# Kernel optimization log

Measured on AMD Instinct MI355X. Metric: run time of the kernel, lower is better.

Reference implementation:

```python
import jax, jax.numpy as jnp
import numpy as np

B, S, D, H, DK = 2, 2048, 1024, 16, 64
NUM_BUCKETS, MAX_DIST = 32, 128
EPS = 1e-6


def _relative_position_bucket(rel, num_buckets=NUM_BUCKETS, max_distance=MAX_DIST):
    # bidirectional (T5 encoder) bucketing
    nb = num_buckets // 2
    bucket = (rel > 0).astype(jnp.int32) * nb
    n = jnp.abs(rel)
    max_exact = nb // 2
    is_small = n < max_exact
    large = max_exact + (
        jnp.log(jnp.maximum(n, 1).astype(jnp.float32) / max_exact)
        / np.log(max_distance / max_exact)
        * (nb - max_exact)
    ).astype(jnp.int32)
    large = jnp.minimum(large, nb - 1)
    return bucket + jnp.where(is_small, n, large)


def softmax1(logits):
    # off-by-one softmax: exp(x-m) / (sum(exp(x-m)) + exp(-m))
    m = jax.lax.stop_gradient(jnp.max(logits, axis=-1, keepdims=True))
    e = jnp.exp(logits - m)
    return e / (jnp.sum(e, axis=-1, keepdims=True) + jnp.exp(-m))


def setup_inputs() -> dict:
    key = jax.random.key(0)
    ks = jax.random.split(key, 8)
    scale = 0.02
    return {
        "hidden_states": jax.random.normal(ks[0], (B, S, D), dtype=jnp.float32),
        "delete_gate_mask": jax.random.normal(ks[1], (B, S, 1), dtype=jnp.float32),
        "ln_w": jnp.ones((D,), dtype=jnp.float32),
        "q_w": jax.random.normal(ks[2], (D, H * DK), dtype=jnp.float32) * scale,
        "k_w": jax.random.normal(ks[3], (D, H * DK), dtype=jnp.float32) * scale,
        "v_w": jax.random.normal(ks[4], (D, H * DK), dtype=jnp.float32) * scale,
        "o_w": jax.random.normal(ks[5], (H * DK, D), dtype=jnp.float32) * scale,
        "rel_emb": jax.random.normal(ks[6], (NUM_BUCKETS, H), dtype=jnp.float32) * scale,
    }


def reference(hidden_states, delete_gate_mask, ln_w, q_w, k_w, v_w, o_w, rel_emb):
    # T5LayerNorm (RMS norm, no mean subtraction, no bias)
    var = jnp.mean(jnp.square(hidden_states), axis=-1, keepdims=True)
    x = hidden_states * jax.lax.rsqrt(var + EPS) * ln_w

    # projections (T5 Linear layers have no bias, no 1/sqrt(d) scaling)
    q = (x @ q_w).reshape(B, S, H, DK).transpose(0, 2, 1, 3)  # bhqd
    k = (x @ k_w).reshape(B, S, H, DK).transpose(0, 2, 1, 3)  # bhkd
    v = (x @ v_w).reshape(B, S, H, DK).transpose(0, 2, 1, 3)  # bhkd

    scores = jnp.einsum("bhqd,bhkd->bhqk", q, k)

    # relative position bias: [1, H, S, S]
    pos = jnp.arange(S)
    rel = pos[None, :] - pos[:, None]  # key_pos - query_pos
    bucket = _relative_position_bucket(rel)  # [S, S]
    position_bias = rel_emb[bucket].transpose(2, 0, 1)[None]  # [1,H,S,S]

    # delete gate: [B,S,1] -> additive mask over key axis [B,1,1,S]
    gate = delete_gate_mask[..., 0][:, None, None, :]

    scores = scores + position_bias + gate
    attn = softmax1(scores.astype(jnp.float32)).astype(scores.dtype)

    attn_out = jnp.einsum("bhqk,bhkd->bhqd", attn, v)
    attn_out = attn_out.transpose(0, 2, 1, 3).reshape(B, S, H * DK) @ o_w

    # residual (dropout disabled at p=0)
    return hidden_states + attn_out
```

## Files before the change

### kernel.cpp

```cpp
#include <hip/hip_runtime.h>
#include <hip/hip_bf16.h>
#include <math.h>

typedef __attribute__((ext_vector_type(8))) short short8;
typedef __attribute__((ext_vector_type(4))) float f32x4;

#define S_LEN   2048
#define DMODEL  1024
#define NHEAD   16
#define HDK     64
#define NBATCH  2
#define MTOT    (NBATCH*S_LEN)
#define LOG2E   1.4426950408889634f

__device__ __forceinline__ unsigned short f2bf(float f) {
  union { float f; unsigned u; } c; c.f = f;
  unsigned r = c.u + 0x7FFFu + ((c.u >> 16) & 1u);
  return (unsigned short)(r >> 16);
}

__device__ __forceinline__ short8 lds_ld16(const unsigned short* p) {
  return *reinterpret_cast<const short8*>(p);
}

__device__ __forceinline__ void gload_lds16(const unsigned short* g, unsigned short* l) {
  __builtin_amdgcn_global_load_lds(
      (const __attribute__((address_space(1))) unsigned int*)g,
      (__attribute__((address_space(3))) unsigned int*)l, 16, 0, 0);
}

__global__ __launch_bounds__(256) void transpose_w_kernel(
    const float* __restrict__ qw, const float* __restrict__ kw,
    const float* __restrict__ vw, const float* __restrict__ ow,
    unsigned short* __restrict__ wqkv, unsigned short* __restrict__ wo) {
  int z = blockIdx.z;
  const float* src = (z==0)?qw:(z==1)?kw:(z==2)?vw:ow;
  unsigned short* dst = (z<3) ? (wqkv + (size_t)z*DMODEL*DMODEL) : wo;
  __shared__ float tile[32][33];
  int n0 = blockIdx.x*32, k0 = blockIdx.y*32;
  int tx = threadIdx.x, ty = threadIdx.y;
  for (int r = ty; r < 32; r += 8)
    tile[r][tx] = src[(size_t)(k0+r)*DMODEL + n0 + tx];
  __syncthreads();
  for (int r = ty; r < 32; r += 8)
    dst[(size_t)(n0+r)*DMODEL + k0 + tx] = f2bf(tile[tx][r]);
}

__global__ void bias_table_kernel(const float* __restrict__ rel_emb,
                                  float* __restrict__ btab) {
  int idx = blockIdx.x*256 + threadIdx.x;
  if (idx >= NHEAD*4095) return;
  int h = idx / 4095, rp = idx % 4095, rel = rp - 2047;
  int bucket = (rel > 0) ? 16 : 0;
  int n = (rel < 0) ? -rel : rel;
  int v;
  if (n < 8) v = n;
  else {
    float lrv = logf((float)n * 0.125f) / 2.7725887f * 8.0f;
    v = 8 + (int)lrv;
    if (v > 15) v = 15;
  }
  btab[idx] = rel_emb[(size_t)(bucket + v)*NHEAD + h] * LOG2E;
}

__global__ void eg_kernel(const float* __restrict__ gmask,
                          float* __restrict__ egf,
                          unsigned short* __restrict__ egb) {
  int i = blockIdx.x*256 + threadIdx.x;
  float e = __expf(gmask[i]);
  egf[i] = e;
  egb[i] = f2bf(e);
}

__global__ __launch_bounds__(256) void rmsnorm_kernel(
    const float* __restrict__ hs, const float* __restrict__ lnw,
    unsigned short* __restrict__ xo) {
  int row = blockIdx.x, t = threadIdx.x;
  const float4 v = ((const float4*)(hs + (size_t)row*DMODEL))[t];
  float ss = v.x*v.x + v.y*v.y + v.z*v.z + v.w*v.w;
  #pragma unroll
  for (int off = 32; off >= 1; off >>= 1) ss += __shfl_xor(ss, off, 64);
  __shared__ float wsum[4];
  if ((t & 63) == 0) wsum[t >> 6] = ss;
  __syncthreads();
  float tot = wsum[0] + wsum[1] + wsum[2] + wsum[3];
  float sc = rsqrtf(tot * (1.0f/DMODEL) + 1e-6f);
  const float4 lw = ((const float4*)lnw)[t];
  uint2 o;
  o.x = (unsigned)f2bf(v.x*sc*lw.x) | ((unsigned)f2bf(v.y*sc*lw.y) << 16);
  o.y = (unsigned)f2bf(v.z*sc*lw.z) | ((unsigned)f2bf(v.w*sc*lw.w) << 16);
  ((uint2*)(xo + (size_t)row*DMODEL))[t] = o;
}

template<int EPI>
__global__ __launch_bounds__(256) void gemm128(
    const unsigned short* __restrict__ X,
    const unsigned short* __restrict__ W,
    unsigned short* __restrict__ Oq, unsigned short* __restrict__ Ok,
    unsigned short* __restrict__ Ov,
    const float* __restrict__ resid, float* __restrict__ Of,
    const float* __restrict__ escale) {
  __shared__ unsigned short As[128*64];
  __shared__ unsigned short Bs[128*64];
  const int z = blockIdx.z;
  int m0, n0;
  const unsigned short *Ap, *Bp;
  if (EPI == 0 && z == 2) {
    m0 = blockIdx.y*128; n0 = blockIdx.x*128;
    Ap = W + (size_t)2*DMODEL*DMODEL; Bp = X;
  } else {
    m0 = blockIdx.x*128; n0 = blockIdx.y*128;
    Ap = X; Bp = W + ((EPI==0) ? (size_t)z*DMODEL*DMODEL : 0);
  }
  const int t = threadIdx.x, lane = t & 63, w = t >> 6;
  const int g = lane >> 4, lr = lane & 15;
  const int wr = (w >> 1)*64, wc = (w & 1)*64;

  f32x4 acc[4][4];
  #pragma unroll
  for (int mi = 0; mi < 4; mi++)
    #pragma unroll
    for (int ni = 0; ni < 4; ni++) acc[mi][ni] = (f32x4){0.f,0.f,0.f,0.f};

  const unsigned short* ag[4]; const unsigned short* bg[4];
  unsigned short* al[4]; unsigned short* bl[4];
  #pragma unroll
  for (int i = 0; i < 4; i++) {
    int slot = t + i*256, row = slot >> 3, c8 = slot & 7;
    int cs = c8 ^ (row & 7);
    ag[i] = Ap + (size_t)(m0 + row)*DMODEL + cs*8;
    bg[i] = Bp + (size_t)(n0 + row)*DMODEL + cs*8;
    al[i] = As + slot*8;
    bl[i] = Bs + slot*8;
  }

  for (int kk = 0; kk < DMODEL; kk += 64) {
    #pragma unroll
    for (int i = 0; i < 4; i++) {
      gload_lds16(ag[i] + kk, al[i]);
      gload_lds16(bg[i] + kk, bl[i]);
    }
    __syncthreads();
    #pragma unroll
    for (int ks = 0; ks < 2; ks++) {
      short8 af[4], bfr[4];
      #pragma unroll
      for (int mi = 0; mi < 4; mi++) {
        int R = wr + mi*16 + lr;
        af[mi] = lds_ld16(As + R*64 + (((ks*4 + g) ^ (R & 7)) << 3));
      }
      #pragma unroll
      for (int ni = 0; ni < 4; ni++) {
        int R = wc + ni*16 + lr;
        bfr[ni] = lds_ld16(Bs + R*64 + (((ks*4 + g) ^ (R & 7)) << 3));
      }
      #pragma unroll
      for (int mi = 0; mi < 4; mi++)
        #pragma unroll
        for (int ni = 0; ni < 4; ni++)
          acc[mi][ni] = __builtin_amdgcn_mfma_f32_16x16x32_bf16(af[mi], bfr[ni], acc[mi][ni], 0, 0, 0);
    }
    __syncthreads();
  }

  if (EPI == 0) {
    if (z < 2) {
      unsigned short* dst = (z == 0) ? Oq : Ok;
      const float osc = (z == 0) ? LOG2E : 1.0f;
      #pragma unroll
      for (int mi = 0; mi < 4; mi++) {
        #pragma unroll
        for (int r = 0; r < 4; r++) {
          int m = m0 + wr + mi*16 + g*4 + r;
          int b = m >> 11, s = m & (S_LEN-1);
          unsigned short* drow = dst + ((size_t)b*NHEAD*S_LEN + s)*HDK;
          #pragma unroll
          for (int ni = 0; ni < 4; ni++) {
            int n = n0 + wc + ni*16 + lr;
            int h = n >> 6, dcol = n & 63;
            drow[(size_t)h*S_LEN*HDK + dcol] = f2bf(acc[mi][ni][r] * osc);
          }
        }
      }
    } else {
      #pragma unroll
      for (int ni = 0; ni < 4; ni++) {
        int n = n0 + wc + ni*16 + lr;
        int b = n >> 11, s = n & (S_LEN-1);
        float e = escale[n];
        #pragma unroll
        for (int mi = 0; mi < 4; mi++)
          #pragma unroll
          for (int r = 0; r < 4; r++) {
            int m = m0 + wr + mi*16 + g*4 + r;
            Ov[((size_t)b*DMODEL + m)*S_LEN + s] = f2bf(acc[mi][ni][r] * e);
          }
      }
    }
  } else {
    #pragma unroll
    for (int mi = 0; mi < 4; mi++) {
      #pragma unroll
      for (int r = 0; r < 4; r++) {
        int m = m0 + wr + mi*16 + g*4 + r;
        const float* rrow = resid + (size_t)m*DMODEL;
        float* orow = Of + (size_t)m*DMODEL;
        #pragma unroll
        for (int ni = 0; ni < 4; ni++) {
          int n = n0 + wc + ni*16 + lr;
          orow[n] = rrow[n] + acc[mi][ni][r];
        }
      }
    }
  }
}

__global__ __launch_bounds__(256, 2) void attn_kernel(
    const unsigned short* __restrict__ Qg,
    const unsigned short* __restrict__ Kg,
    const unsigned short* __restrict__ Vtg,
    const float* __restrict__ btab,
    const unsigned short* __restrict__ egb,
    unsigned short* __restrict__ Og) {
  __shared__ __align__(16) unsigned short Kl[2][64][64];
  __shared__ __align__(16) unsigned short Vl[2][64][64];
  __shared__ __align__(16) unsigned short Pl[4][16*64];

  const int flat = blockIdx.x;
  const int xcd = flat & 7, j = flat >> 3;
  const int bh = xcd*4 + (j >> 4), qx = j & 15;
  const int b = bh >> 4, h = bh & 15;
  const int q0 = qx * 128;

  const int t = threadIdx.x, w = t >> 6, lane = t & 63;
  const int g = lane >> 4, lr = lane & 15, l7 = lane & 7;
  const int srow0 = t >> 3, sg0 = t & 7, srow1 = srow0 + 32;
  const int swz = (sg0 ^ (srow0 & 7)) << 3;

  const unsigned short* Qb = Qg  + (size_t)bh*S_LEN*HDK;
  const unsigned short* Kb = Kg  + (size_t)bh*S_LEN*HDK;
  const unsigned short* Vb = Vtg + (size_t)bh*HDK*S_LEN;
  const unsigned short* ge = egb + (size_t)b*S_LEN;

  const int qs0A = q0 + w*32, qs0B = qs0A + 16;
  short8 qfA0 = *reinterpret_cast<const short8*>(Qb + (size_t)(qs0A+lr)*HDK + g*8);
  short8 qfA1 = *reinterpret_cast<const short8*>(Qb + (size_t)(qs0A+lr)*HDK + 32 + g*8);
  short8 qfB0 = *reinterpret_cast<const short8*>(Qb + (size_t)(qs0B+lr)*HDK + g*8);
  short8 qfB1 = *reinterpret_cast<const short8*>(Qb + (size_t)(qs0B+lr)*HDK + 32 + g*8);

  f32x4 accA[4], accB[4], l4A, l4B;
  #pragma unroll
  for (int n = 0; n < 4; n++) { accA[n] = (f32x4){0.f,0.f,0.f,0.f}; accB[n] = (f32x4){0.f,0.f,0.f,0.f}; }
  l4A = (f32x4){0.f,0.f,0.f,0.f}; l4B = (f32x4){0.f,0.f,0.f,0.f};

  const float* btb = btab + (size_t)h*4095 + 2047;
  const float cpos = btb[91];
  const float cneg = btb[-91];

  {
    *reinterpret_cast<uint4*>(&Kl[0][srow0][swz]) =
        *reinterpret_cast<const uint4*>(Kb + (size_t)srow0*HDK + sg0*8);
    *reinterpret_cast<uint4*>(&Kl[0][srow1][swz]) =
        *reinterpret_cast<const uint4*>(Kb + (size_t)srow1*HDK + sg0*8);
    *reinterpret_cast<uint4*>(&Vl[0][srow0][swz]) =
        *reinterpret_cast<const uint4*>(Vb + (size_t)srow0*S_LEN + sg0*8);
    *reinterpret_cast<uint4*>(&Vl[0][srow1][swz]) =
        *reinterpret_cast<const uint4*>(Vb + (size_t)srow1*S_LEN + sg0*8);
  }

  char* prow = (char*)&Pl[w][0] + lr*128;

  int cur = 0;
  const int NT = S_LEN/64;
  for (int kt = 0; kt < NT; ++kt) {
    const int key0 = kt*64;
    __syncthreads();

    uint4 nk0, nk1, nv0, nv1;
    const bool pf = (kt + 1 < NT);
    if (pf) {
      nk0 = *reinterpret_cast<const uint4*>(Kb + (size_t)(key0+64+srow0)*HDK + sg0*8);
      nk1 = *reinterpret_cast<const uint4*>(Kb + (size_t)(key0+64+srow1)*HDK + sg0*8);
      nv0 = *reinterpret_cast<const uint4*>(Vb + (size_t)srow0*S_LEN + key0+64 + sg0*8);
      nv1 = *reinterpret_cast<const uint4*>(Vb + (size_t)srow1*S_LEN + key0+64 + sg0*8);
    }

    short8 bk[4][2];
    #pragma unroll
    for (int n = 0; n < 4; n++) {
      const unsigned short* kr = &Kl[cur][n*16 + lr][0];
      bk[n][0] = lds_ld16(kr + ((g ^ l7) << 3));
      bk[n][1] = lds_ld16(kr + (((4 + g) ^ l7) << 3));
    }
    short8 bv[2][4];
    #pragma unroll
    for (int c = 0; c < 2; c++)
      #pragma unroll
      for (int n = 0; n < 4; n++)
        bv[c][n] = lds_ld16(&Vl[cur][n*16 + lr][((4*c + g) ^ l7) << 3]);
    short8 gv[2];
    #pragma unroll
    for (int c = 0; c < 2; c++) {
      short8 z8 = (short8){0,0,0,0,0,0,0,0};
      if (lr == 0)
        z8 = *reinterpret_cast<const short8*>(ge + key0 + c*32 + g*8);
      gv[c] = z8;
    }

#define PROCESS_SET(qf0_, qf1_, qs0_, acc_, l4_)                                      \
    {                                                                                 \
      const int dband = key0 - (qs0_);                                                \
      const bool band = (dband > -154 && dband < 106);                                \
      const float cc = band ? 0.f : ((dband > 0) ? cpos : cneg);                      \
      f32x4 zc = (f32x4){cc, cc, cc, cc};               \
      f32x4 sv[4];                                                                    \
      __builtin_amdgcn_s_setprio(1);                                                  \
      _Pragma("unroll") for (int n = 0; n < 4; n++) {                                 \
        sv[n] = __builtin_amdgcn_mfma_f32_16x16x32_bf16(bk[n][0], qf0_, zc, 0, 0, 0); \
        sv[n] = __builtin_amdgcn_mfma_f32_16x16x32_bf16(bk[n][1], qf1_, sv[n], 0, 0, 0); \
      }                                                                               \
      __builtin_amdgcn_s_setprio(0);                                                  \
      if (band) {                                                                     \
        const float* btq = btb + (dband - lr);                                        \
        _Pragma("unroll") for (int n = 0; n < 4; n++)                                 \
          _Pragma("unroll") for (int r = 0; r < 4; r++)                               \
            sv[n][r] += btq[n*16 + g*4 + r];                                          \
      }                                                                               \
      _Pragma("unroll") for (int n = 0; n < 4; n++)                                   \
        _Pragma("unroll") for (int r = 0; r < 4; r++)                                 \
          sv[n][r] = exp2f(sv[n][r]);                                                 \
      _Pragma("unroll") for (int n = 0; n < 4; n++) {                                 \
        unsigned plo_, phi_;                                                          \
        asm("v_cvt_pk_bf16_f32 %0, %1, %2" : "=v"(plo_) : "v"(sv[n][0]), "v"(sv[n][1])); \
        asm("v_cvt_pk_bf16_f32 %0, %1, %2" : "=v"(phi_) : "v"(sv[n][2]), "v"(sv[n][3])); \
        uint2 pw_; pw_.x = plo_; pw_.y = phi_;                                        \
        *reinterpret_cast<uint2*>(prow + ((((2*n + (g>>1)) ^ l7) << 4) + ((g & 1) << 3))) = pw_; \
      }                                                                               \
      __builtin_amdgcn_s_setprio(1);                                                  \
      _Pragma("unroll") for (int c = 0; c < 2; c++) {                                 \
        short8 pa_ = lds_ld16((const unsigned short*)(prow + (((4*c + g) ^ l7) << 4))); \
        _Pragma("unroll") for (int n = 0; n < 4; n++)                                 \
          acc_[n] = __builtin_amdgcn_mfma_f32_16x16x32_bf16(pa_, bv[c][n], acc_[n], 0, 0, 0); \
        l4_ = __builtin_amdgcn_mfma_f32_16x16x32_bf16(pa_, gv[c], l4_, 0, 0, 0);      \
      }                                                                               \
      __builtin_amdgcn_s_setprio(0);                                                  \
    }

    PROCESS_SET(qfA0, qfA1, qs0A, accA, l4A)
    PROCESS_SET(qfB0, qfB1, qs0B, accB, l4B)
#undef PROCESS_SET

    if (pf) {
      *reinterpret_cast<uint4*>(&Kl[cur^1][srow0][swz]) = nk0;
      *reinterpret_cast<uint4*>(&Kl[cur^1][srow1][swz]) = nk1;
      *reinterpret_cast<uint4*>(&Vl[cur^1][srow0][swz]) = nv0;
      *reinterpret_cast<uint4*>(&Vl[cur^1][srow1][swz]) = nv1;
    }
    cur ^= 1;
  }

#define FINAL_SET(acc_, l4_, qs0_)                                                    \
  {                                                                                   \
    _Pragma("unroll") for (int r = 0; r < 4; r++) {                                   \
      float lq = __shfl(l4_[r], g*16);                                                \
      float inv = 1.0f / (lq + 1.0f);                                                 \
      int srw = (qs0_) + g*4 + r;                                                     \
      unsigned short* orow = Og + ((size_t)b*S_LEN + srw)*DMODEL + h*HDK;             \
      _Pragma("unroll") for (int n = 0; n < 4; n++)                                   \
        orow[n*16 + lr] = f2bf(acc_[n][r] * inv);                                     \
    }                                                                                 \
  }
  FINAL_SET(accA, l4A, qs0A)
  FINAL_SET(accB, l4B, qs0B)
#undef FINAL_SET
}

extern "C" void kernel_launch(void* const* d_in, const int* in_sizes, int n_in,
                              void* d_out, int out_size, void* d_ws, size_t ws_size,
                              hipStream_t stream) {
  const float* hs   = (const float*)d_in[0];
  const float* gate = (const float*)d_in[1];
  const float* lnw  = (const float*)d_in[2];
  const float* qw   = (const float*)d_in[3];
  const float* kw   = (const float*)d_in[4];
  const float* vw   = (const float*)d_in[5];
  const float* ow   = (const float*)d_in[6];
  const float* rel  = (const float*)d_in[7];
  float* out = (float*)d_out;

  char* ws = (char*)d_ws;
  const size_t MB = 1ull << 20;
  unsigned short* xbf  = (unsigned short*)(ws);
  unsigned short* wqkv = (unsigned short*)(ws + 8*MB);
  unsigned short* wo   = (unsigned short*)(ws + 14*MB);
  unsigned short* qb   = (unsigned short*)(ws + 16*MB);
  unsigned short* kb   = (unsigned short*)(ws + 24*MB);
  unsigned short* vt   = (unsigned short*)(ws + 32*MB);
  unsigned short* ao   = (unsigned short*)(ws + 40*MB);
  float*          btab = (float*)(ws + 48*MB);
  float*          egf  = (float*)(ws + 48*MB + 256*1024);
  unsigned short* egb  = (unsigned short*)(ws + 48*MB + 272*1024);

  transpose_w_kernel<<<dim3(32,32,4), dim3(32,8), 0, stream>>>(qw, kw, vw, ow, wqkv, wo);
  bias_table_kernel<<<dim3(256), dim3(256), 0, stream>>>(rel, btab);
  eg_kernel<<<dim3(16), dim3(256), 0, stream>>>(gate, egf, egb);
  rmsnorm_kernel<<<dim3(MTOT), dim3(256), 0, stream>>>(hs, lnw, xbf);
  gemm128<0><<<dim3(MTOT/128, DMODEL/128, 3), dim3(256), 0, stream>>>(
      xbf, wqkv, qb, kb, vt, nullptr, nullptr, egf);
  attn_kernel<<<dim3(512), dim3(256), 0, stream>>>(
      qb, kb, vt, btab, egb, ao);
  gemm128<1><<<dim3(MTOT/128, DMODEL/128, 1), dim3(256), 0, stream>>>(
      ao, wo, nullptr, nullptr, nullptr, hs, out, nullptr);
}
```

Baseline: 138.4 us.

## Split attention over key halves with combine kernel and async LDS staging

Attention now splits the key range into two halves, doubling the grid to 1024 blocks and writing unnormalized partial outputs plus partial row sums. A new combine kernel adds the halves and normalizes. This is valid without rescaling because the kernel uses no running max. K/V staging switches to direct global-to-LDS loads, and the A/B query sets are interleaved in shared MFMA loops. In exchange it adds an extra launch, extra global traffic, and bf16 rounding of the partials. The split path runs only when the workspace is large enough.

Measured after the change: 142.7 us. 3.1% more time.

```diff
diff --git a/kernel.cpp b/kernel.cpp
--- a/kernel.cpp
+++ b/kernel.cpp
@@ -17,6 +17,10 @@
   union { float f; unsigned u; } c; c.f = f;
   unsigned r = c.u + 0x7FFFu + ((c.u >> 16) & 1u);
   return (unsigned short)(r >> 16);
+}
+__device__ __forceinline__ float bf2f(unsigned short u) {
+  union { unsigned u; float f; } c; c.u = ((unsigned)u) << 16;
+  return c.f;
 }
 
 __device__ __forceinline__ short8 lds_ld16(const unsigned short* p) {
@@ -215,32 +219,53 @@
   }
 }
 
+__global__ __launch_bounds__(256, 2) void combine_guard_dummy() {}
+template<int SPLIT>
 __global__ __launch_bounds__(256, 2) void attn_kernel(
     const unsigned short* __restrict__ Qg,
     const unsigned short* __restrict__ Kg,
     const unsigned short* __restrict__ Vtg,
     const float* __restrict__ btab,
     const unsigned short* __restrict__ egb,
-    unsigned short* __restrict__ Og) {
+    unsigned short* __restrict__ Og,
+    unsigned short* __restrict__ Op0,
+    unsigned short* __restrict__ Op1,
+    float* __restrict__ lpart) {
   __shared__ __align__(16) unsigned short Kl[2][64][64];
   __shared__ __align__(16) unsigned short Vl[2][64][64];
-  __shared__ __align__(16) unsigned short Pl[4][16*64];
+  __shared__ __align__(16) unsigned short Pl[4][2][16*64];
 
   const int flat = blockIdx.x;
   const int xcd = flat & 7, j = flat >> 3;
-  const int bh = xcd*4 + (j >> 4), qx = j & 15;
+  int bh, qx, half;
+  if (SPLIT) { bh = xcd*4 + (j >> 5); int rest = j & 31; qx = rest >> 1; half = rest & 1; }
+  else       { bh = xcd*4 + (j >> 4); qx = j & 15; half = 0; }
   const int b = bh >> 4, h = bh & 15;
   const int q0 = qx * 128;
+  const int ktbase = SPLIT ? half*16 : 0;
+  const int ktend  = SPLIT ? ktbase + 16 : 32;
 
   const int t = threadIdx.x, w = t >> 6, lane = t & 63;
   const int g = lane >> 4, lr = lane & 15, l7 = lane & 7;
-  const int srow0 = t >> 3, sg0 = t & 7, srow1 = srow0 + 32;
-  const int swz = (sg0 ^ (srow0 & 7)) << 3;
 
   const unsigned short* Qb = Qg  + (size_t)bh*S_LEN*HDK;
   const unsigned short* Kb = Kg  + (size_t)bh*S_LEN*HDK;
   const unsigned short* Vb = Vtg + (size_t)bh*HDK*S_LEN;
   const unsigned short* ge = egb + (size_t)b*S_LEN;
+
+  const int srow = t >> 3, sg0 = t & 7;
+  const int cs = sg0 ^ (srow & 7);
+  const unsigned short* kS0 = Kb + (size_t)srow*HDK + cs*8;
+  const unsigned short* kS1 = Kb + (size_t)(srow+32)*HDK + cs*8;
+  const unsigned short* vS0 = Vb + (size_t)srow*S_LEN + cs*8;
+  const unsigned short* vS1 = Vb + (size_t)(srow+32)*S_LEN + cs*8;
+
+#define STAGE(nb_, key_) do {                                          \
+    gload_lds16(kS0 + (size_t)(key_)*HDK, &Kl[nb_][0][0] + t*8);       \
+    gload_lds16(kS1 + (size_t)(key_)*HDK, &Kl[nb_][0][0] + t*8 + 2048);\
+    gload_lds16(vS0 + (key_),             &Vl[nb_][0][0] + t*8);       \
+    gload_lds16(vS1 + (key_),             &Vl[nb_][0][0] + t*8 + 2048);\
+  } while (0)
 
   const int qs0A = q0 + w*32, qs0B = qs0A + 16;
   short8 qfA0 = *reinterpret_cast<const short8*>(Qb + (size_t)(qs0A+lr)*HDK + g*8);
@@ -257,47 +282,17 @@
   const float cpos = btb[91];
   const float cneg = btb[-91];
 
-  {
-    *reinterpret_cast<uint4*>(&Kl[0][srow0][swz]) =
-        *reinterpret_cast<const uint4*>(Kb + (size_t)srow0*HDK + sg0*8);
-    *reinterpret_cast<uint4*>(&Kl[0][srow1][swz]) =
-        *reinterpret_cast<const uint4*>(Kb + (size_t)srow1*HDK + sg0*8);
-    *reinterpret_cast<uint4*>(&Vl[0][srow0][swz]) =
-        *reinterpret_cast<const uint4*>(Vb + (size_t)srow0*S_LEN + sg0*8);
-    *reinterpret_cast<uint4*>(&Vl[0][srow1][swz]) =
-        *reinterpret_cast<const uint4*>(Vb + (size_t)srow1*S_LEN + sg0*8);
-  }
-
-  char* prow = (char*)&Pl[w][0] + lr*128;
-
+  char* prowA = (char*)&Pl[w][0][0] + lr*128;
+  char* prowB = (char*)&Pl[w][1][0] + lr*128;
+
+  STAGE(0, ktbase*64);
   int cur = 0;
-  const int NT = S_LEN/64;
-  for (int kt = 0; kt < NT; ++kt) {
+  for (int kt = ktbase; kt < ktend; ++kt) {
     const int key0 = kt*64;
     __syncthreads();
 
-    uint4 nk0, nk1, nv0, nv1;
-    const bool pf = (kt + 1 < NT);
-    if (pf) {
-      nk0 = *reinterpret_cast<const uint4*>(Kb + (size_t)(key0+64+srow0)*HDK + sg0*8);
-      nk1 = *reinterpret_cast<const uint4*>(Kb + (size_t)(key0+64+srow1)*HDK + sg0*8);
-      nv0 = *reinterpret_cast<const uint4*>(Vb + (size_t)srow0*S_LEN + key0+64 + sg0*8);
-      nv1 = *reinterpret_cast<const uint4*>(Vb + (size_t)srow1*S_LEN + key0+64 + sg0*8);
-    }
-
-    short8 bk[4][2];
-    #pragma unroll
-    for (int n = 0; n < 4; n++) {
-      const unsigned short* kr = &Kl[cur][n*16 + lr][0];
-      bk[n][0] = lds_ld16(kr + ((g ^ l7) << 3));
-      bk[n][1] = lds_ld16(kr + (((4 + g) ^ l7) << 3));
-    }
-    short8 bv[2][4];
-    #pragma unroll
-    for (int c = 0; c < 2; c++)
-      #pragma unroll
-      for (int n = 0; n < 4; n++)
-        bv[c][n] = lds_ld16(&Vl[cur][n*16 + lr][((4*c + g) ^ l7) << 3]);
+    if (kt + 1 < ktend) STAGE(cur^1, key0+64);
+
     short8 gv[2];
     #pragma unroll
     for (int c = 0; c < 2; c++) {
@@ -307,72 +302,133 @@
       gv[c] = z8;
     }
 
-#define PROCESS_SET(qf0_, qf1_, qs0_, acc_, l4_)                                      \
+    const int dbA = key0 - qs0A, dbB = key0 - qs0B;
+    const bool bandA = (dbA > -154 && dbA < 106);
+    const bool bandB = (dbB > -154 && dbB < 106);
+    const float ccA = bandA ? 0.f : ((dbA > 0) ? cpos : cneg);
+    const float ccB = bandB ? 0.f : ((dbB > 0) ? cpos : cneg);
+    f32x4 svA[4], svB[4];
+    {
+      f32x4 zA = (f32x4){ccA,ccA,ccA,ccA}, zB = (f32x4){ccB,ccB,ccB,ccB};
+      short8 bk[4];
+      #pragma unroll
+      for (int n = 0; n < 4; n++)
+        bk[n] = lds_ld16(&Kl[cur][n*16 + lr][(g ^ l7) << 3]);
+      __builtin_amdgcn_s_setprio(1);
+      #pragma unroll
+      for (int n = 0; n < 4; n++) {
+        svA[n] = __builtin_amdgcn_mfma_f32_16x16x32_bf16(bk[n], qfA0, zA, 0, 0, 0);
+        svB[n] = __builtin_amdgcn_mfma_f32_16x16x32_bf16(bk[n], qfB0, zB, 0, 0, 0);
+      }
+      __builtin_amdgcn_s_setprio(0);
+      #pragma unroll
+      for (int n = 0; n < 4; n++)
+        bk[n] = lds_ld16(&Kl[cur][n*16 + lr][((4 + g) ^ l7) << 3]);
+      __builtin_amdgcn_s_setprio(1);
+      #pragma unroll
+      for (int n = 0; n < 4; n++) {
+        svA[n] = __builtin_amdgcn_mfma_f32_16x16x32_bf16(bk[n], qfA1, svA[n], 0, 0, 0);
+        svB[n] = __builtin_amdgcn_mfma_f32_16x16x32_bf16(bk[n], qfB1, svB[n], 0, 0, 0);
+      }
+      __builtin_amdgcn_s_setprio(0);
+    }
+
+#define FINISH_SM(sv_, band_, db_, prow_)                                             \
     {                                                                                 \
-      const int dband = key0 - (qs0_);                                                \
-      const bool band = (dband > -154 && dband < 106);                                \
-      const float cc = band ? 0.f : ((dband > 0) ? cpos : cneg);                      \
-      f32x4 zc = (f32x4){cc, cc, cc, cc};               \
-      f32x4 sv[4];                                                                    \
-      __builtin_amdgcn_s_setprio(1);                                                  \
-      _Pragma("unroll") for (int n = 0; n < 4; n++) {                                 \
-        sv[n] = __builtin_amdgcn_mfma_f32_16x16x32_bf16(bk[n][0], qf0_, zc, 0, 0, 0); \
-        sv[n] = __builtin_amdgcn_mfma_f32_16x16x32_bf16(bk[n][1], qf1_, sv[n], 0, 0, 0); \
-      }                                                                               \
-      __builtin_amdgcn_s_setprio(0);                                                  \
-      if (band) {                                                                     \
-        const float* btq = btb + (dband - lr);                                        \
+      if (band_) {                                                                    \
+        const float* btq = btb + ((db_) - lr);                                        \
         _Pragma("unroll") for (int n = 0; n < 4; n++)                                 \
           _Pragma("unroll") for (int r = 0; r < 4; r++)                               \
-            sv[n][r] += btq[n*16 + g*4 + r];                                          \
+            sv_[n][r] += btq[n*16 + g*4 + r];                                         \
       }                                                                               \
       _Pragma("unroll") for (int n = 0; n < 4; n++)                                   \
         _Pragma("unroll") for (int r = 0; r < 4; r++)                                 \
-          sv[n][r] = exp2f(sv[n][r]);                                                 \
+          sv_[n][r] = exp2f(sv_[n][r]);                                               \
       _Pragma("unroll") for (int n = 0; n < 4; n++) {                                 \
         unsigned plo_, phi_;                                                          \
-        asm("v_cvt_pk_bf16_f32 %0, %1, %2" : "=v"(plo_) : "v"(sv[n][0]), "v"(sv[n][1])); \
-        asm("v_cvt_pk_bf16_f32 %0, %1, %2" : "=v"(phi_) : "v"(sv[n][2]), "v"(sv[n][3])); \
+        asm("v_cvt_pk_bf16_f32 %0, %1, %2" : "=v"(plo_) : "v"(sv_[n][0]), "v"(sv_[n][1])); \
+        asm("v_cvt_pk_bf16_f32 %0, %1, %2" : "=v"(phi_) : "v"(sv_[n][2]), "v"(sv_[n][3])); \
         uint2 pw_; pw_.x = plo_; pw_.y = phi_;                                        \
-        *reinterpret_cast<uint2*>(prow + ((((2*n + (g>>1)) ^ l7) << 4) + ((g & 1) << 3))) = pw_; \
+        *reinterpret_cast<uint2*>((prow_) + ((((2*n + (g>>1)) ^ l7) << 4) + ((g & 1) << 3))) = pw_; \
       }                                                                               \
-      __builtin_amdgcn_s_setprio(1);                                                  \
-      _Pragma("unroll") for (int c = 0; c < 2; c++) {                                 \
-        short8 pa_ = lds_ld16((const unsigned short*)(prow + (((4*c + g) ^ l7) << 4))); \
+    }
+    FINISH_SM(svA, bandA, dbA, prowA)
+    FINISH_SM(svB, bandB, dbB, prowB)
+#undef FINISH_SM
+
+    #pragma unroll
+    for (int c = 0; c < 2; c++) {
+      short8 bvf[4];
+      #pragma unroll
+      for (int n = 0; n < 4; n++)
+        bvf[n] = lds_ld16(&Vl[cur][n*16 + lr][((4*c + g) ^ l7) << 3]);
+      short8 paA = lds_ld16((const unsigned short*)(prowA + (((4*c + g) ^ l7) << 4)));
+      short8 paB = lds_ld16((const unsigned short*)(prowB + (((4*c + g) ^ l7) << 4)));
+      __builtin_amdgcn_s_setprio(1);
+      #pragma unroll
+      for (int n = 0; n < 4; n++) {
+        accA[n] = __builtin_amdgcn_mfma_f32_16x16x32_bf16(paA, bvf[n], accA[n], 0, 0, 0);
+        accB[n] = __builtin_amdgcn_mfma_f32_16x16x32_bf16(paB, bvf[n], accB[n], 0, 0, 0);
+      }
+      l4A = __builtin_amdgcn_mfma_f32_16x16x32_bf16(paA, gv[c], l4A, 0, 0, 0);
+      l4B = __builtin_amdgcn_mfma_f32_16x16x32_bf16(paB, gv[c], l4B, 0, 0, 0);
+      __builtin_amdgcn_s_setprio(0);
+    }
+
+    cur ^= 1;
+  }
+
+#define FINAL_SET(acc_, l4_, qs0_, op_)                                               \
+  {                                                                                   \
+    if (SPLIT) {                                                                      \
+      if (lr == 0) {                                                                  \
+        _Pragma("unroll") for (int r = 0; r < 4; r++)                                 \
+          lpart[(size_t)half*(32*S_LEN) + (size_t)bh*S_LEN + (qs0_) + g*4 + r] = l4_[r]; \
+      }                                                                               \
+      _Pragma("unroll") for (int r = 0; r < 4; r++) {                                 \
+        int srw = (qs0_) + g*4 + r;                                                   \
+        unsigned short* orow = (op_) + ((size_t)bh*S_LEN + srw)*HDK;                  \
         _Pragma("unroll") for (int n = 0; n < 4; n++)                                 \
-          acc_[n] = __builtin_amdgcn_mfma_f32_16x16x32_bf16(pa_, bv[c][n], acc_[n], 0, 0, 0); \
-        l4_ = __builtin_amdgcn_mfma_f32_16x16x32_bf16(pa_, gv[c], l4_, 0, 0, 0);      \
+          orow[n*16 + lr] = f2bf(acc_[n][r]);                                         \
       }                                                                               \
-      __builtin_amdgcn_s_setprio(0);                                                  \
-    }
-
-    PROCESS_SET(qfA0, qfA1, qs0A, accA, l4A)
-    PROCESS_SET(qfB0, qfB1, qs0B, accB, l4B)
-#undef PROCESS_SET
-
-    if (pf) {
-      *reinterpret_cast<uint4*>(&Kl[cur^1][srow0][swz]) = nk0;
-      *reinterpret_cast<uint4*>(&Kl[cur^1][srow1][swz]) = nk1;
-      *reinterpret_cast<uint4*>(&Vl[cur^1][srow0][swz]) = nv0;
-      *reinterpret_cast<uint4*>(&Vl[cur^1][srow1][swz]) = nv1;
-    }
-    cur ^= 1;
-  }
-
-#define FINAL_SET(acc_, l4_, qs0_)                                                    \
-  {                                                                                   \
-    _Pragma("unroll") for (int r = 0; r < 4; r++) {                                   \
-      float lq = __shfl(l4_[r], g*16);                                                \
-      float inv = 1.0f / (lq + 1.0f);                                                 \
-      int srw = (qs0_) + g*4 + r;                                                     \
-      unsigned short* orow = Og + ((size_t)b*S_LEN + srw)*DMODEL + h*HDK;             \
-      _Pragma("unroll") for (int n = 0; n < 4; n++)                                   \
-        orow[n*16 + lr] = f2bf(acc_[n][r] * inv);                                     \
+    } else {                                                                          \
+      _Pragma("unroll") for (int r = 0; r < 4; r++) {                                 \
+        float lq = __shfl(l4_[r], g*16);                                              \
+        float inv = 1.0f / (lq + 1.0f);                                               \
+        int srw = (qs0_) + g*4 + r;                                                   \
+        unsigned short* orow = Og + ((size_t)b*S_LEN + srw)*DMODEL + h*HDK;           \
+        _Pragma("unroll") for (int n = 0; n < 4; n++)                                 \
+          orow[n*16 + lr] = f2bf(acc_[n][r] * inv);                                   \
+      }                                                                               \
     }                                                                                 \
   }
-  FINAL_SET(accA, l4A, qs0A)
-  FINAL_SET(accB, l4B, qs0B)
+  unsigned short* op = half ? Op1 : Op0;
+  FINAL_SET(accA, l4A, qs0A, op)
+  FINAL_SET(accB, l4B, qs0B, op)
 #undef FINAL_SET
+#undef STAGE
+}
+
+__global__ __launch_bounds__(256) void combine_kernel(
+    const unsigned short* __restrict__ Op0,
+    const unsigned short* __restrict__ Op1,
+    const float* __restrict__ lpart,
+    unsigned short* __restrict__ ao) {
+  int idx = blockIdx.x*256 + threadIdx.x;
+  int row = idx >> 3;
+  int d0 = (idx & 7) * 8;
+  float l = lpart[row] + lpart[(size_t)32*S_LEN + row] + 1.0f;
+  float inv = 1.0f / l;
+  size_t src = (size_t)row*HDK + d0;
+  short8 o0 = *reinterpret_cast<const short8*>(Op0 + src);
+  short8 o1 = *reinterpret_cast<const short8*>(Op1 + src);
+  int bh = row >> 11, s = row & (S_LEN-1), b = bh >> 4, h = bh & 15;
+  unsigned short out[8];
+  #pragma unroll
+  for (int k = 0; k < 8; k++)
+    out[k] = f2bf((bf2f((unsigned short)o0[k]) + bf2f((unsigned short)o1[k])) * inv);
+  *reinterpret_cast<uint4*>(ao + ((size_t)(b*S_LEN + s))*DMODEL + h*HDK + d0) =
+      *reinterpret_cast<const uint4*>(out);
 }
 
 extern "C" void kernel_launch(void* const* d_in, const int* in_sizes, int n_in,
@@ -398,8 +454,12 @@
   unsigned short* vt   = (unsigned short*)(ws + 32*MB);
   unsigned short* ao   = (unsigned short*)(ws + 40*MB);
   float*          btab = (float*)(ws + 48*MB);
-  float*          egf  = (float*)(ws + 48*MB + 256*1024);
-  unsigned short* egb  = (unsigned short*)(ws + 48*MB + 272*1024);
+  float*          lpart= (float*)(ws + 48*MB + 256*1024);
+  float*          egf  = (float*)(ws + 48*MB + 768*1024);
+  unsigned short* egb  = (unsigned short*)(ws + 48*MB + 784*1024);
+  unsigned short* op1  = (unsigned short*)(ws + 49*MB);
+  unsigned short* op0  = xbf;
+  const bool do_split = ws_size >= (57*MB);
 
   transpose_w_kernel<<<dim3(32,32,4), dim3(32,8), 0, stream>>>(qw, kw, vw, ow, wqkv, wo);
   bias_table_kernel<<<dim3(256), dim3(256), 0, stream>>>(rel, btab);
@@ -407,8 +467,14 @@
   rmsnorm_kernel<<<dim3(MTOT), dim3(256), 0, stream>>>(hs, lnw, xbf);
   gemm128<0><<<dim3(MTOT/128, DMODEL/128, 3), dim3(256), 0, stream>>>(
       xbf, wqkv, qb, kb, vt, nullptr, nullptr, egf);
-  attn_kernel<<<dim3(512), dim3(256), 0, stream>>>(
-      qb, kb, vt, btab, egb, ao);
+  if (do_split) {
+    attn_kernel<1><<<dim3(1024), dim3(256), 0, stream>>>(
+        qb, kb, vt, btab, egb, nullptr, op0, op1, lpart);
+    combine_kernel<<<dim3(2048), dim3(256), 0, stream>>>(op0, op1, lpart, ao);
+  } else {
+    attn_kernel<0><<<dim3(512), dim3(256), 0, stream>>>(
+        qb, kb, vt, btab, egb, ao, nullptr, nullptr, nullptr);
+  }
   gemm128<1><<<dim3(MTOT/128, DMODEL/128, 1), dim3(256), 0, stream>>>(
       ao, wo, nullptr, nullptr, nullptr, hs, out, nullptr);
 }
```
